# Optimization experiments

Measured on AMD Instinct MI355X. Metric: run time of the kernel, lower is better.

Reference implementation:

```python
import jax, jax.numpy as jnp
import numpy as np

N, E, IN, H, L = 50000, 640000, 64, 128, 3
EPS_DIST = 1e-8
LN_EPS = 1e-5


def setup_inputs() -> dict:
    key = jax.random.key(0)
    ks = iter(jax.random.split(key, 64))

    def rn(shape, fan_in):
        return (jax.random.normal(next(ks), shape, jnp.float32) / np.sqrt(fan_in)).astype(jnp.float32)

    inp = {}
    inp['h'] = jax.random.normal(next(ks), (N, IN), jnp.float32)
    inp['x'] = jax.random.normal(next(ks), (N, 3), jnp.float32)
    inp['edge_index'] = jax.random.randint(next(ks), (2, E), 0, N, jnp.int64)
    # embedding_in: Linear(IN, H)
    inp['W_emb'] = rn((IN, H), IN); inp['b_emb'] = jnp.zeros((H,), jnp.float32)
    # per-layer EquivariantConv params, stacked over L
    inp['Wm1'] = rn((L, 2 * H + 1, H), 2 * H + 1); inp['bm1'] = jnp.zeros((L, H), jnp.float32)
    inp['Wm2'] = rn((L, H, H), H);                 inp['bm2'] = jnp.zeros((L, H), jnp.float32)
    inp['Wc1'] = rn((L, H, H), H);                 inp['bc1'] = jnp.zeros((L, H), jnp.float32)
    inp['Wc2'] = rn((L, H, 1), H)  # no bias
    inp['Wn1'] = rn((L, 2 * H, H), 2 * H);         inp['bn1'] = jnp.zeros((L, H), jnp.float32)
    inp['Wn2'] = rn((L, H, H), H);                 inp['bn2'] = jnp.zeros((L, H), jnp.float32)
    inp['ln_g'] = jnp.ones((L, H), jnp.float32);   inp['ln_b'] = jnp.zeros((L, H), jnp.float32)
    # epsilon head params
    inp['Wem1'] = rn((2 * H + 4, H), 2 * H + 4);   inp['bem1'] = jnp.zeros((H,), jnp.float32)
    inp['Wem2'] = rn((H, H), H);                   inp['bem2'] = jnp.zeros((H,), jnp.float32)
    inp['Wec1'] = rn((H, H), H);                   inp['bec1'] = jnp.zeros((H,), jnp.float32)
    inp['Wec2'] = rn((H, 3), H);                   inp['bec2'] = jnp.zeros((3,), jnp.float32)
    inp['Wh1'] = rn((H + 3, H), H + 3);            inp['bh1'] = jnp.zeros((H,), jnp.float32)
    inp['Wh2'] = rn((H, 3), H);                    inp['bh2'] = jnp.zeros((3,), jnp.float32)
    return inp


def _layernorm(v, g, b):
    mu = jnp.mean(v, axis=-1, keepdims=True)
    var = jnp.mean((v - mu) ** 2, axis=-1, keepdims=True)
    return (v - mu) * jax.lax.rsqrt(var + LN_EPS) * g + b


def reference(h, x, edge_index, W_emb, b_emb, Wm1, bm1, Wm2, bm2, Wc1, bc1, Wc2,
              Wn1, bn1, Wn2, bn2, ln_g, ln_b, Wem1, bem1, Wem2, bem2,
              Wec1, bec1, Wec2, bec2, Wh1, bh1, Wh2, bh2):
    row, col = edge_index[0], edge_index[1]
    n = x.shape[0]
    seg = lambda v: jax.ops.segment_sum(v, col, num_segments=n)
    in_degree = seg(jnp.ones((col.shape[0], 1), x.dtype))  # [N,1]

    h = h @ W_emb + b_emb  # embedding_in

    for i in range(L):
        rel = x[row] - x[col]                                   # [E,3]
        dist = jnp.linalg.norm(rel, axis=-1, keepdims=True)     # [E,1]
        mi = jnp.concatenate([h[row], h[col], dist], axis=-1)   # [E,2H+1]
        m = jax.nn.silu(jax.nn.silu(mi @ Wm1[i] + bm1[i]) @ Wm2[i] + bm2[i])
        agg = seg(m)                                            # [N,H]
        rel_dir = rel / (dist + EPS_DIST)
        coord_mult = jnp.tanh(jax.nn.silu(m @ Wc1[i] + bc1[i]) @ Wc2[i])  # [E,1]
        coord_update = seg(coord_mult * rel_dir)                # [N,3]
        x = x + coord_update / (in_degree + 1.0)
        nu = jnp.concatenate([h, agg], axis=-1)
        h = h + jax.nn.silu(nu @ Wn1[i] + bn1[i]) @ Wn2[i] + bn2[i]
        h = _layernorm(h, ln_g[i], ln_b[i])

    # predict_epsilon (eps_directional_head=False, eps_use_local_head=True, eps_normalize_agg=False)
    rel = x[row] - x[col]
    dist = jnp.linalg.norm(rel, axis=-1, keepdims=True)
    mi = jnp.concatenate([h[row], h[col], rel, dist], axis=-1)  # [E,2H+4]
    em = jax.nn.silu(jax.nn.silu(mi @ Wem1 + bem1) @ Wem2 + bem2)
    eps_src = jax.nn.silu(em @ Wec1 + bec1) @ Wec2 + bec2       # [E,3]
    eps = seg(eps_src)                                          # [N,3]
    hx = jnp.concatenate([h, x], axis=-1)
    eps = eps + jax.nn.silu(hx @ Wh1 + bh1) @ Wh2 + bh2
    return (h, x, eps)
```

## Files before the change

kernel.cpp:

```cpp
#include <hip/hip_runtime.h>

#define N_NODES 50000
#define N_EDGES 640000
#define HDIM    128
#define NLAYERS 3

typedef __attribute__((ext_vector_type(4))) float f32x4;
typedef short s16x8 __attribute__((ext_vector_type(8)));
typedef __bf16 bf16v8 __attribute__((ext_vector_type(8)));

static __device__ __forceinline__ unsigned short f2b(float f){
  unsigned int u = __float_as_uint(f);
  unsigned int r = u + 0x7FFFu + ((u >> 16) & 1u);
  return (unsigned short)(r >> 16);
}
static __device__ __forceinline__ float b2f(unsigned short h){
  return __uint_as_float(((unsigned int)h) << 16);
}
static __device__ __forceinline__ float silu_f(float x){
  return x / (1.0f + __expf(-x));
}
static __device__ __forceinline__ unsigned int cvt2(float a, float b){
  unsigned int r;
  asm("v_cvt_pk_bf16_f32 %0, %1, %2" : "=v"(r) : "v"(a), "v"(b));
// ... 22 lines not shown
  r[4]=(short)b.x; r[5]=(short)b.y; r[6]=(short)b.z; r[7]=(short)b.w;
  return r;
}
static __device__ __forceinline__ s16x8 ldBf32(const float* __restrict__ p, int q){
  float4 a = *(const float4*)(p + (q<<2));
  float4 b = *(const float4*)(p + 16 + (q<<2));
  s16x8 r;
  r[0]=(short)f2b(a.x); r[1]=(short)f2b(a.y); r[2]=(short)f2b(a.z); r[3]=(short)f2b(a.w);
  r[4]=(short)f2b(b.x); r[5]=(short)f2b(b.y); r[6]=(short)f2b(b.z); r[7]=(short)f2b(b.w);
  return r;
}

#define GLL(SRC, DST) __builtin_amdgcn_global_load_lds( \
    (const __attribute__((address_space(1))) void*)(SRC), \
    (__attribute__((address_space(3))) void*)(DST), 16, 0, 0)
#define STG2(T0,BUF) do{ \
    const unsigned short* _s = blob + (((size_t)(T0))<<12) + (w<<11) + (lane<<3); \
    unsigned char* _d = &sm.wbuf[BUF][(w<<12) + (lane<<4)]; \
    GLL(_s, _d); GLL(_s+512, _d+1024); GLL(_s+1024, _d+2048); GLL(_s+1536, _d+3072); \
  }while(0)
#define STG1(T0,BUF) do{ \
    const unsigned short* _s = blob + (((size_t)(T0))<<12) + (w<<10) + (lane<<3); \
    unsigned char* _d = &sm.wbuf[BUF][(w<<11) + (lane<<4)]; \
    GLL(_s, _d); GLL(_s+512, _d+1024); \
  }while(0)
#define WAITV(N) asm volatile("s_waitcnt vmcnt(" #N ")" ::: "memory")
#define BARF do{ __builtin_amdgcn_s_barrier(); asm volatile("" ::: "memory"); }while(0)
#define EBAR do{ asm volatile("" ::: "memory"); __builtin_amdgcn_s_barrier(); }while(0)

#define PH2(BUF, BEXPR, ACC) do{ \
  _Pragma("unroll") for (int ti=0; ti<2; ++ti){ \
    _Pragma("unroll") for (int s=0;s<8;++s){ \
      const s16x8 _A = *(const s16x8*)&sm.wbuf[BUF][(ti<<13)+(s<<10)+toff]; \
      _Pragma("unroll") for (int e=0;e<4;++e) ACC[e][s] = MFMA(_A, (BEXPR), ACC[e][s]); \
    } } }while(0)
#define PH1(BUF, BEXPR, ACC) do{ \
  _Pragma("unroll") for (int s=0;s<8;++s){ \
    const s16x8 _A = *(const s16x8*)&sm.wbuf[BUF][(s<<10)+toff]; \
    _Pragma("unroll") for (int e=0;e<4;++e) ACC[e][s] = MFMA(_A, (BEXPR), ACC[e][s]); \
  } }while(0)

__global__ void k_conv(const float* __restrict__ W, unsigned short* __restrict__ WT, int kshift){
  const int K = 1 << kshift;
  const int idx = (blockIdx.x<<8) + threadIdx.x;
  if (idx < (K<<7)){
    const int n = idx >> kshift;
    const int k = idx & (K-1);
    WT[idx] = f2b(W[(size_t)k*HDIM + n]);
  }
}

__global__ void k_conv_blob(const float* __restrict__ W1, const float* __restrict__ W2,
                            const float* __restrict__ W3, const float* __restrict__ aux,
                            const float* __restrict__ bias, int naux,
                            unsigned short* __restrict__ blob){
  const int i = (blockIdx.x<<8) + threadIdx.x;
  if (i >= 17*4096) return;
  const int t = i >> 12;
  const int n = (i >> 5) & 127;
  const int slot = (i >> 3) & 3;
  const int j = i & 7;
  const int q = slot ^ ((n >> 1) & 3);
  const int kl = ((j >> 2) << 4) + (q << 2) + (j & 3);
  float v;
  if (t == 0)      v = (kl < naux) ? aux[(size_t)kl*HDIM + n] : (kl == 16 ? bias[n] : 0.f);
  else if (t < 9)  v = W1[(size_t)(((t-1)<<5)+kl)*HDIM + n];
  else if (t < 13) v = W2[(size_t)(((t-9)<<5)+kl)*HDIM + n];
  else             v = W3[(size_t)(((t-13)<<5)+kl)*HDIM + n];
  blob[i] = f2b(v);
}

__global__ void k_degree(const int* __restrict__ coli, int* __restrict__ degi){
  const int e = (blockIdx.x<<8) + threadIdx.x;
  if (e < N_EDGES) atomicAdd(&degi[coli[e]], 1);
}
__global__ void k_scanA(const int* __restrict__ degi, int* __restrict__ off, int* __restrict__ bsum){
  const int t = threadIdx.x, b = blockIdx.x;
  const int i = (b<<8) + t;
  const int v = (i < N_NODES) ? degi[i] : 0;
  int x = v;
  const int lane = t & 63;
  #pragma unroll
  for (int d=1; d<64; d<<=1){ int y = __shfl_up(x, d); if (lane >= d) x += y; }
  __shared__ int wsum[4];
// ... 24 lines not shown
}
__global__ void k_scanC(int* __restrict__ off, const int* __restrict__ bsum, int* __restrict__ cursor){
  const int i = (blockIdx.x<<8) + threadIdx.x;
  if (i < N_NODES){
    const int o = off[i] + bsum[i>>8];
    off[i] = o;
    cursor[i] = o;
  }
}
__global__ void k_fill(const int* __restrict__ coli, int* __restrict__ cursor, int* __restrict__ perm){
  const int e = (blockIdx.x<<8) + threadIdx.x;
  if (e < N_EDGES){
    const int p = atomicAdd(&cursor[coli[e]], 1);
    perm[e] = p;
  }
}
__global__ void k_xcopy(const float* __restrict__ xin, float* __restrict__ xbuf){
  const int i = (blockIdx.x<<8) + threadIdx.x;
  if (i < N_NODES*3) xbuf[i] = xin[i];
}

__global__ __launch_bounds__(256) void k_embed(
    const float* __restrict__ hin, const unsigned short* __restrict__ WembT,
    const float* __restrict__ bemb, float* __restrict__ hbuf,
    unsigned short* __restrict__ hb)
{
  __shared__ float s_b[128];
  const int tid = threadIdx.x;
  if (tid < 128) s_b[tid] = bemb[tid];
  __syncthreads();
  const int lane = tid & 63, q = lane>>4;
  const int n = (blockIdx.x<<6) + ((tid>>6)<<4) + (lane&15);
  const bool valid = n < N_NODES;
  const int nc = valid ? n : (N_NODES-1);
// ... 11 lines not shown
  }
  if (valid){
    float* op = hbuf + (size_t)n*HDIM;
    unsigned short* hbw = hb + (size_t)n*HDIM;
    #pragma unroll
    for (int s=0;s<8;++s){
      float4 o; o.x=acc[s][0]; o.y=acc[s][1]; o.z=acc[s][2]; o.w=acc[s][3];
      *(float4*)(op + (s<<4) + (q<<2)) = o;
      ushort4 u; u.x=f2b(o.x); u.y=f2b(o.y); u.z=f2b(o.z); u.w=f2b(o.w);
      *(ushort4*)(hbw + ((s>>1)<<5) + (q<<3) + ((s&1)<<2)) = u;
    }
  }
}

template<bool CSR>
__global__ __launch_bounds__(256,2) void k_edge_mlp(
    const unsigned short* __restrict__ hb, const float* __restrict__ xbuf,
    const int* __restrict__ rowi, const int* __restrict__ coli,
    const int* __restrict__ perm, const unsigned short* __restrict__ blob,
    const float* __restrict__ bm2v, const float* __restrict__ bc1v,
    const float* __restrict__ wc2v,
    unsigned short* __restrict__ m_buf, float* __restrict__ agg,
    float* __restrict__ cu)
{
  __shared__ struct {
    alignas(16) unsigned char wbuf[2][16384];
    int row[256], col[256], prm[256];
    float dist[256]; float rdir[256][3];
    float b2[128], bc1[128], wc2[128];
  } sm;
  const int tid = threadIdx.x, lane = tid & 63, w = tid >> 6, q = lane >> 4;
  const int q8 = q << 3;
  const int ebase = blockIdx.x << 8;
  {
    const int e = ebase + tid;
    const int r = rowi[e], c = coli[e];
    sm.row[tid] = r; sm.col[tid] = c;
    if (CSR) sm.prm[tid] = perm[e];
    const float dx = xbuf[3*r+0] - xbuf[3*c+0];
    const float dy = xbuf[3*r+1] - xbuf[3*c+1];
    const float dz = xbuf[3*r+2] - xbuf[3*c+2];
    const float d = sqrtf(dx*dx + dy*dy + dz*dz);
    sm.dist[tid] = d;
    const float inv = 1.0f / (d + 1e-8f);
    sm.rdir[tid][0] = dx*inv; sm.rdir[tid][1] = dy*inv; sm.rdir[tid][2] = dz*inv;
  }
  if (tid < 128){ sm.b2[tid]=bm2v[tid]; sm.bc1[tid]=bc1v[tid]; sm.wc2[tid]=wc2v[tid]; }
  STG2(0,0); STG2(2,1);
  __syncthreads();

  const int toff = ((lane&15)<<6) + ((q ^ ((lane>>1)&3))<<4);
  int rn[4], cn[4];
  #pragma unroll
  for (int e=0;e<4;++e){
    const int el = (w<<6) + (e<<4) + (lane&15);
    rn[e] = sm.row[el]; cn[e] = sm.col[el];
  }
  s16x8 BA[4][2], BB[4][2];
  #pragma unroll
  for (int e=0;e<4;++e){
    const int el = (w<<6) + (e<<4) + (lane&15);
    s16x8 bx = {0,0,0,0,0,0,0,0};
    if (q == 0){ bx[0] = (short)f2b(sm.dist[el]); bx[4] = (short)0x3F80; }
    BA[e][0] = bx;
    BA[e][1] = *(const s16x8*)(hb + ((size_t)rn[e]<<7) + q8);
  }
  f32x4 acc[4][8] = {};

  BARF;
  #pragma unroll
  for (int e=0;e<4;++e){
    BB[e][0] = *(const s16x8*)(hb + ((size_t)rn[e]<<7) + 32 + q8);
    BB[e][1] = *(const s16x8*)(hb + ((size_t)rn[e]<<7) + 64 + q8);
  }
  PH2(0, BA[e][ti], acc);
  EBAR; STG2(4,0);
  BARF;
  #pragma unroll
  for (int e=0;e<4;++e){
    BA[e][0] = *(const s16x8*)(hb + ((size_t)rn[e]<<7) + 96 + q8);
    BA[e][1] = *(const s16x8*)(hb + ((size_t)cn[e]<<7) + q8);
  }
  PH2(1, BB[e][ti], acc);
  EBAR; STG2(6,1);
  WAITV(12); BARF;
  #pragma unroll
  for (int e=0;e<4;++e){
    BB[e][0] = *(const s16x8*)(hb + ((size_t)cn[e]<<7) + 32 + q8);
    BB[e][1] = *(const s16x8*)(hb + ((size_t)cn[e]<<7) + 64 + q8);
  }
  PH2(0, BA[e][ti], acc);
  EBAR; STG1(8,0);
  WAITV(10); BARF;
  #pragma unroll
  for (int e=0;e<4;++e)
    BA[e][0] = *(const s16x8*)(hb + ((size_t)cn[e]<<7) + 96 + q8);
  PH2(1, BB[e][ti], acc);
  EBAR; STG2(9,1);
  WAITV(8); BARF;
  PH1(0, BA[e][0], acc);
  EBAR; STG2(11,0);

  s16x8 sb[4][4];
  #pragma unroll
  for (int e=0;e<4;++e)
    #pragma unroll
    for (int c=0;c<4;++c) sb[e][c] = siluPack(acc[e][2*c], acc[e][2*c+1]);
  f32x4 acc2[4][8];
  #pragma unroll
  for (int s=0;s<8;++s){
    const f32x4 b = *(const f32x4*)&sm.b2[(s<<4)+(q<<2)];
    #pragma unroll
    for (int e=0;e<4;++e) acc2[e][s] = b;
  }
  WAITV(4); BARF;
  PH2(1, sb[e][ti], acc2);
  EBAR; STG2(13,1);
  WAITV(4); BARF;
  PH2(0, sb[e][2+ti], acc2);
  EBAR; STG2(15,0);

  s16x8 mb[4][4];
  #pragma unroll
  for (int e=0;e<4;++e)
    #pragma unroll
    for (int c=0;c<4;++c) mb[e][c] = siluPack(acc2[e][2*c], acc2[e][2*c+1]);
  f32x4 acc3[4][8];
  #pragma unroll
  for (int s=0;s<8;++s){
    const f32x4 b = *(const f32x4*)&sm.bc1[(s<<4)+(q<<2)];
    #pragma unroll
    for (int e=0;e<4;++e) acc3[e][s] = b;
  }
  WAITV(4); BARF;
  PH2(1, mb[e][ti], acc3);
  EBAR;
  WAITV(0); BARF;
  PH2(0, mb[e][2+ti], acc3);

  float dot[4] = {0.f,0.f,0.f,0.f};
  #pragma unroll
  for (int s=0;s<8;++s){
    const f32x4 wv = *(const f32x4*)&sm.wc2[(s<<4)+(q<<2)];
    #pragma unroll
    for (int e=0;e<4;++e)
      #pragma unroll
      for (int r=0;r<4;++r) dot[e] += silu_f(acc3[e][s][r]) * wv[r];
  }
  #pragma unroll
  for (int e=0;e<4;++e){
    dot[e] += __shfl_xor(dot[e], 16);
    dot[e] += __shfl_xor(dot[e], 32);
    const float cm = tanhf(dot[e]);
    const int el = (w<<6) + (e<<4) + (lane&15);
    if (q < 3) atomicAdd(&cu[(size_t)cn[e]*3 + q], cm * sm.rdir[el][q]);
  }
  if (CSR){
    #pragma unroll
    for (int e=0;e<4;++e){
      const int el = (w<<6) + (e<<4) + (lane&15);
      unsigned short* mp = m_buf + ((size_t)sm.prm[el]<<7) + q8;
      #pragma unroll
      for (int c=0;c<4;++c) *(s16x8*)(mp + (c<<5)) = mb[e][c];
    }
  } else {
    #pragma unroll
    for (int e=0;e<4;++e){
      float* ap = agg + (size_t)cn[e]*HDIM + (q<<2);
      #pragma unroll
      for (int c=0;c<4;++c)
        #pragma unroll
        for (int j=0;j<8;++j){
          const int o = (((c<<1)+(j>>2))<<4) + (j&3);
          atomicAdd(ap + o, b2f((unsigned short)mb[e][c][j]));
        }
    }
  }
}

template<bool CSR>
__global__ __launch_bounds__(256) void k_node_mlp(
    float* __restrict__ hbuf, unsigned short* __restrict__ hb,
    float* __restrict__ xbuf,
    const unsigned short* __restrict__ m_buf, const float* __restrict__ agg,
    const int* __restrict__ off, const int* __restrict__ degi,
    const float* __restrict__ cu,
    const unsigned short* __restrict__ Wn1T, const float* __restrict__ bn1v,
    const unsigned short* __restrict__ Wn2T, const float* __restrict__ bn2v,
    const float* __restrict__ lng, const float* __restrict__ lnb)
{
  __shared__ float s_bn1[128], s_bn2[128], s_g[128], s_b[128];
  const int tid = threadIdx.x;
  const int nbase = blockIdx.x << 6;
  if (tid >= 128){
    const int f = tid - 128;
    s_bn1[f]=bn1v[f]; s_bn2[f]=bn2v[f]; s_g[f]=lng[f]; s_b[f]=lnb[f];
  } else if (tid < 64){
    const int n = nbase + tid;
    if (n < N_NODES){
      const float dd = (float)degi[n] + 1.0f;
      #pragma unroll
      for (int c=0;c<3;++c) xbuf[3*n+c] += cu[3*n+c] / dd;
    }
  }
  __syncthreads();

  const int lane = tid & 63, q = lane >> 4;
  const int q8 = q << 3;
  const int n = nbase + ((tid>>6)<<4) + (lane & 15);
  const bool valid = (n < N_NODES);
  const int nc = valid ? n : (N_NODES-1);
  const float* __restrict__ hp = hbuf + (size_t)nc*HDIM;
  const unsigned short* __restrict__ hbp = hb + (size_t)nc*HDIM;

  float aggv[4][8];
  #pragma unroll
  for (int kk=0;kk<4;++kk)
// ... 84 lines not shown
    #pragma unroll
    for (int s=0;s<8;++s){
      const int f0 = (s<<4)+(q<<2);
      float4 o;
      o.x = (v[s][0]-mu)*rs*s_g[f0+0] + s_b[f0+0];
      o.y = (v[s][1]-mu)*rs*s_g[f0+1] + s_b[f0+1];
      o.z = (v[s][2]-mu)*rs*s_g[f0+2] + s_b[f0+2];
      o.w = (v[s][3]-mu)*rs*s_g[f0+3] + s_b[f0+3];
      *(float4*)(op + f0) = o;
      ushort4 u; u.x=f2b(o.x); u.y=f2b(o.y); u.z=f2b(o.z); u.w=f2b(o.w);
      *(ushort4*)(hbw + ((s>>1)<<5) + q8 + ((s&1)<<2)) = u;
    }
  }
}

__global__ __launch_bounds__(256,2) void k_eps_edge(
    const unsigned short* __restrict__ hb, const float* __restrict__ xbuf,
    const int* __restrict__ rowi, const int* __restrict__ coli,
    const unsigned short* __restrict__ blob,
    const float* __restrict__ bem2v, const float* __restrict__ bec1v,
    const float* __restrict__ Wec2, const float* __restrict__ bec2,
    float* __restrict__ epsb)
{
  __shared__ struct {
    alignas(16) unsigned char wbuf[2][16384];
    int row[256], col[256];
    float rel[256][3]; float dist[256];
    float b2[128], bc1[128], wc[3][128];
  } sm;
  const int tid = threadIdx.x, lane = tid & 63, w = tid >> 6, q = lane >> 4;
  const int q8 = q << 3;
  const int ebase = blockIdx.x << 8;
  {
    const int e = ebase + tid;
    const int r = rowi[e], c = coli[e];
    sm.row[tid]=r; sm.col[tid]=c;
    const float dx = xbuf[3*r+0]-xbuf[3*c+0];
    const float dy = xbuf[3*r+1]-xbuf[3*c+1];
    const float dz = xbuf[3*r+2]-xbuf[3*c+2];
    sm.rel[tid][0]=dx; sm.rel[tid][1]=dy; sm.rel[tid][2]=dz;
    sm.dist[tid] = sqrtf(dx*dx+dy*dy+dz*dz);
  }
  if (tid < 128){
    sm.b2[tid]=bem2v[tid]; sm.bc1[tid]=bec1v[tid];
    sm.wc[0][tid]=Wec2[tid*3+0]; sm.wc[1][tid]=Wec2[tid*3+1]; sm.wc[2][tid]=Wec2[tid*3+2];
  }
  STG2(0,0); STG2(2,1);
  __syncthreads();

  const int toff = ((lane&15)<<6) + ((q ^ ((lane>>1)&3))<<4);
  int rn[4], cn[4];
  #pragma unroll
  for (int e=0;e<4;++e){
    const int el = (w<<6) + (e<<4) + (lane&15);
    rn[e] = sm.row[el]; cn[e] = sm.col[el];
  }
  s16x8 BA[4][2], BB[4][2];
  #pragma unroll
  for (int e=0;e<4;++e){
    const int el = (w<<6) + (e<<4) + (lane&15);
    s16x8 bx = {0,0,0,0,0,0,0,0};
    if (q == 0){
      bx[0] = (short)f2b(sm.rel[el][0]);
      bx[1] = (short)f2b(sm.rel[el][1]);
      bx[2] = (short)f2b(sm.rel[el][2]);
      bx[3] = (short)f2b(sm.dist[el]);
      bx[4] = (short)0x3F80;
    }
    BA[e][0] = bx;
    BA[e][1] = *(const s16x8*)(hb + ((size_t)rn[e]<<7) + q8);
  }
  f32x4 acc[4][8] = {};

  BARF;
  #pragma unroll
  for (int e=0;e<4;++e){
    BB[e][0] = *(const s16x8*)(hb + ((size_t)rn[e]<<7) + 32 + q8);
    BB[e][1] = *(const s16x8*)(hb + ((size_t)rn[e]<<7) + 64 + q8);
  }
  PH2(0, BA[e][ti], acc);
  EBAR; STG2(4,0);
  BARF;
  #pragma unroll
  for (int e=0;e<4;++e){
    BA[e][0] = *(const s16x8*)(hb + ((size_t)rn[e]<<7) + 96 + q8);
    BA[e][1] = *(const s16x8*)(hb + ((size_t)cn[e]<<7) + q8);
  }
  PH2(1, BB[e][ti], acc);
  EBAR; STG2(6,1);
  WAITV(12); BARF;
  #pragma unroll
  for (int e=0;e<4;++e){
    BB[e][0] = *(const s16x8*)(hb + ((size_t)cn[e]<<7) + 32 + q8);
    BB[e][1] = *(const s16x8*)(hb + ((size_t)cn[e]<<7) + 64 + q8);
  }
  PH2(0, BA[e][ti], acc);
  EBAR; STG1(8,0);
  WAITV(10); BARF;
  #pragma unroll
  for (int e=0;e<4;++e)
    BA[e][0] = *(const s16x8*)(hb + ((size_t)cn[e]<<7) + 96 + q8);
  PH2(1, BB[e][ti], acc);
  EBAR; STG2(9,1);
  WAITV(8); BARF;
  PH1(0, BA[e][0], acc);
  EBAR; STG2(11,0);

  s16x8 sb[4][4];
  #pragma unroll
  for (int e=0;e<4;++e)
    #pragma unroll
    for (int c=0;c<4;++c) sb[e][c] = siluPack(acc[e][2*c], acc[e][2*c+1]);
  f32x4 acc2[4][8];
  #pragma unroll
  for (int s=0;s<8;++s){
    const f32x4 b = *(const f32x4*)&sm.b2[(s<<4)+(q<<2)];
    #pragma unroll
    for (int e=0;e<4;++e) acc2[e][s] = b;
  }
  WAITV(4); BARF;
  PH2(1, sb[e][ti], acc2);
  EBAR; STG2(13,1);
  WAITV(4); BARF;
  PH2(0, sb[e][2+ti], acc2);
  EBAR; STG2(15,0);

  s16x8 mb[4][4];
  #pragma unroll
  for (int e=0;e<4;++e)
    #pragma unroll
    for (int c=0;c<4;++c) mb[e][c] = siluPack(acc2[e][2*c], acc2[e][2*c+1]);
  f32x4 acc3[4][8];
  #pragma unroll
  for (int s=0;s<8;++s){
    const f32x4 b = *(const f32x4*)&sm.bc1[(s<<4)+(q<<2)];
    #pragma unroll
    for (int e=0;e<4;++e) acc3[e][s] = b;
  }
  WAITV(4); BARF;
  PH2(1, mb[e][ti], acc3);
  EBAR;
  WAITV(0); BARF;
  PH2(0, mb[e][2+ti], acc3);

  float d0[4]={0,0,0,0}, d1[4]={0,0,0,0}, d2[4]={0,0,0,0};
  #pragma unroll
  for (int s=0;s<8;++s){
    const f32x4 w0 = *(const f32x4*)&sm.wc[0][(s<<4)+(q<<2)];
    const f32x4 w1 = *(const f32x4*)&sm.wc[1][(s<<4)+(q<<2)];
    const f32x4 w2 = *(const f32x4*)&sm.wc[2][(s<<4)+(q<<2)];
    #pragma unroll
    for (int e=0;e<4;++e)
      #pragma unroll
      for (int r=0;r<4;++r){
        const float ev = silu_f(acc3[e][s][r]);
        d0[e] += ev*w0[r]; d1[e] += ev*w1[r]; d2[e] += ev*w2[r];
      }
  }
  #pragma unroll
  for (int e=0;e<4;++e){
    d0[e] += __shfl_xor(d0[e],16); d0[e] += __shfl_xor(d0[e],32);
    d1[e] += __shfl_xor(d1[e],16); d1[e] += __shfl_xor(d1[e],32);
    d2[e] += __shfl_xor(d2[e],16); d2[e] += __shfl_xor(d2[e],32);
    if (q < 3){
      const float val = (q==0)?d0[e]:((q==1)?d1[e]:d2[e]);
// ... 98 lines not shown
  float* hbuf = (float*)d_out;
  float* xbuf = hbuf + (size_t)N_NODES*HDIM;
  float* epsb = xbuf + (size_t)N_NODES*3;

  char* wp = (char*)d_ws;
  auto alloc = [&](size_t bytes)->char*{
    char* p = wp; wp += (bytes + 255) & ~(size_t)255; return p;
  };
  unsigned short* WembT = (unsigned short*)alloc((size_t)128*64*2);
  unsigned short *Wn1T[NLAYERS], *Wn2T[NLAYERS];
  for (int i=0;i<NLAYERS;++i){
    Wn1T[i] = (unsigned short*)alloc((size_t)128*256*2);
    Wn2T[i] = (unsigned short*)alloc((size_t)128*128*2);
  }
  unsigned short* Wh1T  = (unsigned short*)alloc((size_t)128*128*2);
  unsigned short* blobL = (unsigned short*)alloc((size_t)NLAYERS*17*4096*2);
  unsigned short* blobE = (unsigned short*)alloc((size_t)17*4096*2);
  unsigned short* hb    = (unsigned short*)alloc((size_t)N_NODES*HDIM*2);
  int* degi   = (int*)alloc((size_t)N_NODES*4);
  int* offv   = (int*)alloc((size_t)N_NODES*4);
  int* cursor = (int*)alloc((size_t)N_NODES*4);
  int* bsum   = (int*)alloc(4096);
  float* cu   = (float*)alloc((size_t)N_NODES*3*4);
  int* perm   = (int*)alloc((size_t)N_EDGES*4);
  char* big   = alloc((size_t)N_EDGES*HDIM*2);
  const bool use_csr = ((size_t)(wp - (char*)d_ws) <= ws_size);
  unsigned short* m_buf = (unsigned short*)big;
  float* agg = (float*)big;

  auto conv = [&](const float* W, unsigned short* WT, int kshift){
    const int tot = 128 << kshift;
    k_conv<<<dim3((tot+255)/256), dim3(256), 0, stream>>>(W, WT, kshift);
  };
  conv(W_emb, WembT, 6);
  for (int i=0;i<NLAYERS;++i){
    conv(Wn1 + (size_t)i*256*128, Wn1T[i], 8);
    conv(Wn2 + (size_t)i*128*128, Wn2T[i], 7);
  }
  conv(Wh1,  Wh1T,  7);
  const int cb_grid = (17*4096)/256;
  for (int i=0;i<NLAYERS;++i){
    const float* Wm1i = Wm1 + (size_t)i*257*128;
    k_conv_blob<<<dim3(cb_grid), dim3(256), 0, stream>>>(
        Wm1i, Wm2 + (size_t)i*128*128, Wc1 + (size_t)i*128*128,
        Wm1i + (size_t)256*128, bm1 + i*128, 1, blobL + (size_t)i*17*4096);
  }
  k_conv_blob<<<dim3(cb_grid), dim3(256), 0, stream>>>(
      Wem1, Wem2, Wec1, Wem1 + (size_t)256*128, bem1, 4, blobE);

  hipMemsetAsync(degi, 0, (size_t)N_NODES*4, stream);
  k_degree<<<dim3((N_EDGES+255)/256), dim3(256), 0, stream>>>(coli, degi);
  const int nb = (N_NODES + 255)/256;
  if (use_csr){
    k_scanA<<<dim3(nb), dim3(256), 0, stream>>>(degi, offv, bsum);
    k_scanB<<<dim3(1), dim3(256), 0, stream>>>(bsum, nb);
    k_scanC<<<dim3(nb), dim3(256), 0, stream>>>(offv, bsum, cursor);
    k_fill<<<dim3((N_EDGES+255)/256), dim3(256), 0, stream>>>(coli, cursor, perm);
  }
  k_xcopy<<<dim3((N_NODES*3+255)/256), dim3(256), 0, stream>>>(x_in, xbuf);
  k_embed<<<dim3((N_NODES+63)/64), dim3(256), 0, stream>>>(h_in, WembT, b_emb, hbuf, hb);

  for (int i=0;i<NLAYERS;++i){
    hipMemsetAsync(cu, 0, (size_t)N_NODES*3*4, stream);
    if (!use_csr) hipMemsetAsync(agg, 0, (size_t)N_NODES*HDIM*4, stream);
    const unsigned short* blob_i = blobL + (size_t)i*17*4096;
    if (use_csr){
      k_edge_mlp<true><<<dim3(N_EDGES/256), dim3(256), 0, stream>>>(
        hb, xbuf, rowi, coli, perm, blob_i,
        bm2 + i*128, bc1 + i*128, Wc2 + i*128, m_buf, agg, cu);
      k_node_mlp<true><<<dim3((N_NODES+63)/64), dim3(256), 0, stream>>>(
        hbuf, hb, xbuf, m_buf, agg, offv, degi, cu,
        Wn1T[i], bn1 + i*128, Wn2T[i], bn2 + i*128, lng + i*128, lnb + i*128);
    } else {
      k_edge_mlp<false><<<dim3(N_EDGES/256), dim3(256), 0, stream>>>(
        hb, xbuf, rowi, coli, perm, blob_i,
        bm2 + i*128, bc1 + i*128, Wc2 + i*128, m_buf, agg, cu);
      k_node_mlp<false><<<dim3((N_NODES+63)/64), dim3(256), 0, stream>>>(
        hbuf, hb, xbuf, m_buf, agg, offv, degi, cu,
        Wn1T[i], bn1 + i*128, Wn2T[i], bn2 + i*128, lng + i*128, lnb + i*128);
    }
  }
  hipMemsetAsync(epsb, 0, (size_t)N_NODES*3*4, stream);
  k_eps_edge<<<dim3(N_EDGES/256), dim3(256), 0, stream>>>(
    hb, xbuf, rowi, coli, blobE, bem2, bec1, Wec2, bec2, epsb);
  k_eps_node<<<dim3((N_NODES+63)/64), dim3(256), 0, stream>>>(
    hbuf, xbuf, Wh1T, bh1, Wh1 + (size_t)128*128, Wh2, bh2, epsb);
}
```

Baseline: 1.264 ms.

## Stage full weight blob in LDS once per 512-edge block and batch setup kernels

The edge MLP kernels now load all 16 weight tiles (128 KB) into LDS in one go at block start instead of double-buffering 16 KB chunks with many barriers. Blocks grow to 512 threads covering 512 edges, so the weight staging is shared by more edges. The distance and relative-position terms become FP32 bias initialisation instead of an extra MFMA K-tile. Setup work is batched: the conversion kernels and memsets are merged into multi-job launches and an init kernel, and the node kernel clears cu after using it. The large LDS footprint limits blocks per CU, which may reduce occupancy and latency hiding for the hb gathers.

```diff
diff --git a/kernel.cpp b/kernel.cpp
--- a/kernel.cpp
+++ b/kernel.cpp
@@ -60,48 +60,25 @@
 #define GLL(SRC, DST) __builtin_amdgcn_global_load_lds( \
     (const __attribute__((address_space(1))) void*)(SRC), \
     (__attribute__((address_space(3))) void*)(DST), 16, 0, 0)
-#define STG2(T0,BUF) do{ \
-    const unsigned short* _s = blob + (((size_t)(T0))<<12) + (w<<11) + (lane<<3); \
-    unsigned char* _d = &sm.wbuf[BUF][(w<<12) + (lane<<4)]; \
-    GLL(_s, _d); GLL(_s+512, _d+1024); GLL(_s+1024, _d+2048); GLL(_s+1536, _d+3072); \
-  }while(0)
-#define STG1(T0,BUF) do{ \
-    const unsigned short* _s = blob + (((size_t)(T0))<<12) + (w<<10) + (lane<<3); \
-    unsigned char* _d = &sm.wbuf[BUF][(w<<11) + (lane<<4)]; \
-    GLL(_s, _d); GLL(_s+512, _d+1024); \
-  }while(0)
-#define WAITV(N) asm volatile("s_waitcnt vmcnt(" #N ")" ::: "memory")
-#define BARF do{ __builtin_amdgcn_s_barrier(); asm volatile("" ::: "memory"); }while(0)
-#define EBAR do{ asm volatile("" ::: "memory"); __builtin_amdgcn_s_barrier(); }while(0)
-
-#define PH2(BUF, BEXPR, ACC) do{ \
-  _Pragma("unroll") for (int ti=0; ti<2; ++ti){ \
-    _Pragma("unroll") for (int s=0;s<8;++s){ \
-      const s16x8 _A = *(const s16x8*)&sm.wbuf[BUF][(ti<<13)+(s<<10)+toff]; \
-      _Pragma("unroll") for (int e=0;e<4;++e) ACC[e][s] = MFMA(_A, (BEXPR), ACC[e][s]); \
-    } } }while(0)
-#define PH1(BUF, BEXPR, ACC) do{ \
-  _Pragma("unroll") for (int s=0;s<8;++s){ \
-    const s16x8 _A = *(const s16x8*)&sm.wbuf[BUF][(s<<10)+toff]; \
-    _Pragma("unroll") for (int e=0;e<4;++e) ACC[e][s] = MFMA(_A, (BEXPR), ACC[e][s]); \
-  } }while(0)
-
-__global__ void k_conv(const float* __restrict__ W, unsigned short* __restrict__ WT, int kshift){
-  const int K = 1 << kshift;
+
+struct ConvJob { const float* src; unsigned short* dst; int kshift; };
+struct ConvJobs { ConvJob j[8]; };
+__global__ void k_conv8(ConvJobs jobs){
+  const ConvJob jb = jobs.j[blockIdx.y];
+  const int K = 1 << jb.kshift;
   const int idx = (blockIdx.x<<8) + threadIdx.x;
   if (idx < (K<<7)){
-    const int n = idx >> kshift;
+    const int n = idx >> jb.kshift;
     const int k = idx & (K-1);
-    WT[idx] = f2b(W[(size_t)k*HDIM + n]);
-  }
-}
-
-__global__ void k_conv_blob(const float* __restrict__ W1, const float* __restrict__ W2,
-                            const float* __restrict__ W3, const float* __restrict__ aux,
-                            const float* __restrict__ bias, int naux,
-                            unsigned short* __restrict__ blob){
+    jb.dst[idx] = f2b(jb.src[(size_t)k*HDIM + n]);
+  }
+}
+
+struct BlobJob { const float *W1, *W2, *W3; unsigned short* dst; };
+struct BlobJobs { BlobJob j[4]; };
+__global__ void k_blob4(BlobJobs jobs){
+  const BlobJob jb = jobs.j[blockIdx.y];
   const int i = (blockIdx.x<<8) + threadIdx.x;
-  if (i >= 17*4096) return;
   const int t = i >> 12;
   const int n = (i >> 5) & 127;
   const int slot = (i >> 3) & 3;
@@ -109,11 +86,18 @@
   const int q = slot ^ ((n >> 1) & 3);
   const int kl = ((j >> 2) << 4) + (q << 2) + (j & 3);
   float v;
-  if (t == 0)      v = (kl < naux) ? aux[(size_t)kl*HDIM + n] : (kl == 16 ? bias[n] : 0.f);
-  else if (t < 9)  v = W1[(size_t)(((t-1)<<5)+kl)*HDIM + n];
-  else if (t < 13) v = W2[(size_t)(((t-9)<<5)+kl)*HDIM + n];
-  else             v = W3[(size_t)(((t-13)<<5)+kl)*HDIM + n];
-  blob[i] = f2b(v);
+  if (t < 8)       v = jb.W1[(size_t)((t<<5)+kl)*HDIM + n];
+  else if (t < 12) v = jb.W2[(size_t)(((t-8)<<5)+kl)*HDIM + n];
+  else             v = jb.W3[(size_t)(((t-12)<<5)+kl)*HDIM + n];
+  jb.dst[i] = f2b(v);
+}
+
+__global__ void k_init(const float* __restrict__ xin, float* __restrict__ xbuf,
+                       float* __restrict__ cu, float* __restrict__ epsb,
+                       int* __restrict__ degi){
+  const int i = (blockIdx.x<<8) + threadIdx.x;
+  if (i < N_NODES*3){ xbuf[i] = xin[i]; cu[i] = 0.f; epsb[i] = 0.f; }
+  if (i < N_NODES) degi[i] = 0;
 }
 
 __global__ void k_degree(const int* __restrict__ coli, int* __restrict__ degi){
@@ -168,10 +152,6 @@
     const int p = atomicAdd(&cursor[coli[e]], 1);
     perm[e] = p;
   }
-}
-__global__ void k_xcopy(const float* __restrict__ xin, float* __restrict__ xbuf){
-  const int i = (blockIdx.x<<8) + threadIdx.x;
-  if (i < N_NODES*3) xbuf[i] = xin[i];
 }
 
 __global__ __launch_bounds__(256) void k_embed(
@@ -213,134 +193,132 @@
 }
 
 template<bool CSR>
-__global__ __launch_bounds__(256,2) void k_edge_mlp(
+__global__ __launch_bounds__(512,2) void k_edge_mlp(
     const unsigned short* __restrict__ hb, const float* __restrict__ xbuf,
     const int* __restrict__ rowi, const int* __restrict__ coli,
     const int* __restrict__ perm, const unsigned short* __restrict__ blob,
+    const float* __restrict__ bm1v, const float* __restrict__ wm1r,
     const float* __restrict__ bm2v, const float* __restrict__ bc1v,
     const float* __restrict__ wc2v,
     unsigned short* __restrict__ m_buf, float* __restrict__ agg,
     float* __restrict__ cu)
 {
-  __shared__ struct {
-    alignas(16) unsigned char wbuf[2][16384];
-    int row[256], col[256], prm[256];
-    float dist[256]; float rdir[256][3];
-    float b2[128], bc1[128], wc2[128];
-  } sm;
-  const int tid = threadIdx.x, lane = tid & 63, w = tid >> 6, q = lane >> 4;
+  __shared__ __align__(16) unsigned char wbuf[16][8192];
+  const int tid = threadIdx.x, lane = tid & 63, q = lane >> 4;
+  const int w = tid >> 6;
   const int q8 = q << 3;
-  const int ebase = blockIdx.x << 8;
-  {
-    const int e = ebase + tid;
-    const int r = rowi[e], c = coli[e];
-    sm.row[tid] = r; sm.col[tid] = c;
-    if (CSR) sm.prm[tid] = perm[e];
-    const float dx = xbuf[3*r+0] - xbuf[3*c+0];
-    const float dy = xbuf[3*r+1] - xbuf[3*c+1];
-    const float dz = xbuf[3*r+2] - xbuf[3*c+2];
+  const int ebase = blockIdx.x << 9;
+
+  #pragma unroll
+  for (int t=0;t<16;++t)
+    GLL(blob + (t<<12) + (tid<<3), &wbuf[t][tid<<4]);
+
+  int rn[4], cn[4], pm[4];
+  float dist[4], rd0[4], rd1[4], rd2[4];
+  #pragma unroll
+  for (int e=0;e<4;++e){
+    const int ge = ebase + (w<<6) + (e<<4) + (lane&15);
+    rn[e] = rowi[ge]; cn[e] = coli[ge];
+    if (CSR) pm[e] = perm[ge];
+    const float dx = xbuf[3*rn[e]+0] - xbuf[3*cn[e]+0];
+    const float dy = xbuf[3*rn[e]+1] - xbuf[3*cn[e]+1];
+    const float dz = xbuf[3*rn[e]+2] - xbuf[3*cn[e]+2];
     const float d = sqrtf(dx*dx + dy*dy + dz*dz);
-    sm.dist[tid] = d;
+    dist[e] = d;
     const float inv = 1.0f / (d + 1e-8f);
-    sm.rdir[tid][0] = dx*inv; sm.rdir[tid][1] = dy*inv; sm.rdir[tid][2] = dz*inv;
-  }
-  if (tid < 128){ sm.b2[tid]=bm2v[tid]; sm.bc1[tid]=bc1v[tid]; sm.wc2[tid]=wc2v[tid]; }
-  STG2(0,0); STG2(2,1);
+    rd0[e] = dx*inv; rd1[e] = dy*inv; rd2[e] = dz*inv;
+  }
+
+  f32x4 acc[4][8];
+  #pragma unroll
+  for (int s=0;s<8;++s){
+    const f32x4 b1 = *(const f32x4*)&bm1v[(s<<4)+(q<<2)];
+    const f32x4 wv = *(const f32x4*)&wm1r[(s<<4)+(q<<2)];
+    #pragma unroll
+    for (int e=0;e<4;++e)
+      #pragma unroll
+      for (int r=0;r<4;++r) acc[e][s][r] = b1[r] + dist[e]*wv[r];
+  }
+  const int toff = ((lane&15)<<6) + ((q ^ ((lane>>1)&3))<<4);
+
+  s16x8 Bc[4];
+  #pragma unroll
+  for (int e=0;e<4;++e)
+    Bc[e] = *(const s16x8*)(hb + ((size_t)rn[e]<<7) + q8);
+
   __syncthreads();
 
-  const int toff = ((lane&15)<<6) + ((q ^ ((lane>>1)&3))<<4);
-  int rn[4], cn[4];
-  #pragma unroll
-  for (int e=0;e<4;++e){
-    const int el = (w<<6) + (e<<4) + (lane&15);
-    rn[e] = sm.row[el]; cn[e] = sm.col[el];
-  }
-  s16x8 BA[4][2], BB[4][2];
-  #pragma unroll
-  for (int e=0;e<4;++e){
-    const int el = (w<<6) + (e<<4) + (lane&15);
-    s16x8 bx = {0,0,0,0,0,0,0,0};
-    if (q == 0){ bx[0] = (short)f2b(sm.dist[el]); bx[4] = (short)0x3F80; }
-    BA[e][0] = bx;
-    BA[e][1] = *(const s16x8*)(hb + ((size_t)rn[e]<<7) + q8);
-  }
-  f32x4 acc[4][8] = {};
-
-  BARF;
-  #pragma unroll
-  for (int e=0;e<4;++e){
-    BB[e][0] = *(const s16x8*)(hb + ((size_t)rn[e]<<7) + 32 + q8);
-    BB[e][1] = *(const s16x8*)(hb + ((size_t)rn[e]<<7) + 64 + q8);
-  }
-  PH2(0, BA[e][ti], acc);
-  EBAR; STG2(4,0);
-  BARF;
-  #pragma unroll
-  for (int e=0;e<4;++e){
-    BA[e][0] = *(const s16x8*)(hb + ((size_t)rn[e]<<7) + 96 + q8);
-    BA[e][1] = *(const s16x8*)(hb + ((size_t)cn[e]<<7) + q8);
-  }
-  PH2(1, BB[e][ti], acc);
-  EBAR; STG2(6,1);
-  WAITV(12); BARF;
-  #pragma unroll
-  for (int e=0;e<4;++e){
-    BB[e][0] = *(const s16x8*)(hb + ((size_t)cn[e]<<7) + 32 + q8);
-    BB[e][1] = *(const s16x8*)(hb + ((size_t)cn[e]<<7) + 64 + q8);
-  }
-  PH2(0, BA[e][ti], acc);
-  EBAR; STG1(8,0);
-  WAITV(10); BARF;
+  #pragma unroll
+  for (int kk=0;kk<8;++kk){
+    s16x8 Bn[4];
+    if (kk < 7){
+      const int k1 = kk+1;
+      #pragma unroll
+      for (int e=0;e<4;++e){
+        const int node = (k1 < 4) ? rn[e] : cn[e];
+        Bn[e] = *(const s16x8*)(hb + ((size_t)node<<7) + ((k1&3)<<5) + q8);
+      }
+    }
+    #pragma unroll
+    for (int s=0;s<8;++s){
+      const s16x8 A = *(const s16x8*)&wbuf[kk][(s<<10)+toff];
+      #pragma unroll
+      for (int e=0;e<4;++e) acc[e][s] = MFMA(A, Bc[e], acc[e][s]);
+    }
+    if (kk < 7){
+      #pragma unroll
+      for (int e=0;e<4;++e) Bc[e] = Bn[e];
+    }
+  }
+
+  s16x8 sb[4][4];
   #pragma unroll
   for (int e=0;e<4;++e)
-    BA[e][0] = *(const s16x8*)(hb + ((size_t)cn[e]<<7) + 96 + q8);
-  PH2(1, BB[e][ti], acc);
-  EBAR; STG2(9,1);
-  WAITV(8); BARF;
-  PH1(0, BA[e][0], acc);
-  EBAR; STG2(11,0);
-
-  s16x8 sb[4][4];
+    #pragma unroll
+    for (int c=0;c<4;++c) sb[e][c] = siluPack(acc[e][2*c], acc[e][2*c+1]);
+
+  f32x4 acc2[4][8];
+  #pragma unroll
+  for (int s=0;s<8;++s){
+    const f32x4 b = *(const f32x4*)&bm2v[(s<<4)+(q<<2)];
+    #pragma unroll
+    for (int e=0;e<4;++e) acc2[e][s] = b;
+  }
+  #pragma unroll
+  for (int c=0;c<4;++c)
+    #pragma unroll
+    for (int s=0;s<8;++s){
+      const s16x8 A = *(const s16x8*)&wbuf[8+c][(s<<10)+toff];
+      #pragma unroll
+      for (int e=0;e<4;++e) acc2[e][s] = MFMA(A, sb[e][c], acc2[e][s]);
+    }
+
+  s16x8 mb[4][4];
   #pragma unroll
   for (int e=0;e<4;++e)
     #pragma unroll
-    for (int c=0;c<4;++c) sb[e][c] = siluPack(acc[e][2*c], acc[e][2*c+1]);
-  f32x4 acc2[4][8];
+    for (int c=0;c<4;++c) mb[e][c] = siluPack(acc2[e][2*c], acc2[e][2*c+1]);
+
+  f32x4 acc3[4][8];
   #pragma unroll
   for (int s=0;s<8;++s){
-    const f32x4 b = *(const f32x4*)&sm.b2[(s<<4)+(q<<2)];
-    #pragma unroll
-    for (int e=0;e<4;++e) acc2[e][s] = b;
-  }
-  WAITV(4); BARF;
-  PH2(1, sb[e][ti], acc2);
-  EBAR; STG2(13,1);
-  WAITV(4); BARF;
-  PH2(0, sb[e][2+ti], acc2);
-  EBAR; STG2(15,0);
-
-  s16x8 mb[4][4];
-  #pragma unroll
-  for (int e=0;e<4;++e)
-    #pragma unroll
-    for (int c=0;c<4;++c) mb[e][c] = siluPack(acc2[e][2*c], acc2[e][2*c+1]);
-  f32x4 acc3[4][8];
+    const f32x4 b = *(const f32x4*)&bc1v[(s<<4)+(q<<2)];
+    #pragma unroll
+    for (int e=0;e<4;++e) acc3[e][s] = b;
+  }
+  #pragma unroll
+  for (int c=0;c<4;++c)
+    #pragma unroll
+    for (int s=0;s<8;++s){
+      const s16x8 A = *(const s16x8*)&wbuf[12+c][(s<<10)+toff];
+      #pragma unroll
+      for (int e=0;e<4;++e) acc3[e][s] = MFMA(A, mb[e][c], acc3[e][s]);
+    }
+
+  float dot[4] = {0.f,0.f,0.f,0.f};
   #pragma unroll
   for (int s=0;s<8;++s){
-    const f32x4 b = *(const f32x4*)&sm.bc1[(s<<4)+(q<<2)];
-    #pragma unroll
-    for (int e=0;e<4;++e) acc3[e][s] = b;
-  }
-  WAITV(4); BARF;
-  PH2(1, mb[e][ti], acc3);
-  EBAR;
-  WAITV(0); BARF;
-  PH2(0, mb[e][2+ti], acc3);
-
-  float dot[4] = {0.f,0.f,0.f,0.f};
-  #pragma unroll
-  for (int s=0;s<8;++s){
-    const f32x4 wv = *(const f32x4*)&sm.wc2[(s<<4)+(q<<2)];
+    const f32x4 wv = *(const f32x4*)&wc2v[(s<<4)+(q<<2)];
     #pragma unroll
     for (int e=0;e<4;++e)
       #pragma unroll
@@ -351,14 +329,15 @@
     dot[e] += __shfl_xor(dot[e], 16);
     dot[e] += __shfl_xor(dot[e], 32);
     const float cm = tanhf(dot[e]);
-    const int el = (w<<6) + (e<<4) + (lane&15);
-    if (q < 3) atomicAdd(&cu[(size_t)cn[e]*3 + q], cm * sm.rdir[el][q]);
+    if (q < 3){
+      const float rdq = (q==0) ? rd0[e] : ((q==1) ? rd1[e] : rd2[e]);
+      atomicAdd(&cu[(size_t)cn[e]*3 + q], cm * rdq);
+    }
   }
   if (CSR){
     #pragma unroll
     for (int e=0;e<4;++e){
-      const int el = (w<<6) + (e<<4) + (lane&15);
-      unsigned short* mp = m_buf + ((size_t)sm.prm[el]<<7) + q8;
+      unsigned short* mp = m_buf + ((size_t)pm[e]<<7) + q8;
       #pragma unroll
       for (int c=0;c<4;++c) *(s16x8*)(mp + (c<<5)) = mb[e][c];
     }
@@ -383,7 +362,7 @@
     float* __restrict__ xbuf,
     const unsigned short* __restrict__ m_buf, const float* __restrict__ agg,
     const int* __restrict__ off, const int* __restrict__ degi,
-    const float* __restrict__ cu,
+    float* __restrict__ cu,
     const unsigned short* __restrict__ Wn1T, const float* __restrict__ bn1v,
     const unsigned short* __restrict__ Wn2T, const float* __restrict__ bn2v,
     const float* __restrict__ lng, const float* __restrict__ lnb)
@@ -399,7 +378,10 @@
     if (n < N_NODES){
       const float dd = (float)degi[n] + 1.0f;
       #pragma unroll
-      for (int c=0;c<3;++c) xbuf[3*n+c] += cu[3*n+c] / dd;
+      for (int c=0;c<3;++c){
+        xbuf[3*n+c] += cu[3*n+c] / dd;
+        cu[3*n+c] = 0.f;
+      }
     }
   }
   __syncthreads();
@@ -514,141 +496,142 @@
   }
 }
 
-__global__ __launch_bounds__(256,2) void k_eps_edge(
+__global__ __launch_bounds__(512,2) void k_eps_edge(
     const unsigned short* __restrict__ hb, const float* __restrict__ xbuf,
     const int* __restrict__ rowi, const int* __restrict__ coli,
     const unsigned short* __restrict__ blob,
+    const float* __restrict__ bem1v, const float* __restrict__ wem_rows,
     const float* __restrict__ bem2v, const float* __restrict__ bec1v,
     const float* __restrict__ Wec2, const float* __restrict__ bec2,
     float* __restrict__ epsb)
 {
-  __shared__ struct {
-    alignas(16) unsigned char wbuf[2][16384];
-    int row[256], col[256];
-    float rel[256][3]; float dist[256];
-    float b2[128], bc1[128], wc[3][128];
-  } sm;
-  const int tid = threadIdx.x, lane = tid & 63, w = tid >> 6, q = lane >> 4;
+  __shared__ __align__(16) unsigned char wbuf[16][8192];
+  __shared__ float wcs[3][128];
+  const int tid = threadIdx.x, lane = tid & 63, q = lane >> 4;
+  const int w = tid >> 6;
   const int q8 = q << 3;
-  const int ebase = blockIdx.x << 8;
-  {
-    const int e = ebase + tid;
-    const int r = rowi[e], c = coli[e];
-    sm.row[tid]=r; sm.col[tid]=c;
-    const float dx = xbuf[3*r+0]-xbuf[3*c+0];
-    const float dy = xbuf[3*r+1]-xbuf[3*c+1];
-    const float dz = xbuf[3*r+2]-xbuf[3*c+2];
-    sm.rel[tid][0]=dx; sm.rel[tid][1]=dy; sm.rel[tid][2]=dz;
-    sm.dist[tid] = sqrtf(dx*dx+dy*dy+dz*dz);
-  }
+  const int ebase = blockIdx.x << 9;
+
+  #pragma unroll
+  for (int t=0;t<16;++t)
+    GLL(blob + (t<<12) + (tid<<3), &wbuf[t][tid<<4]);
   if (tid < 128){
-    sm.b2[tid]=bem2v[tid]; sm.bc1[tid]=bec1v[tid];
-    sm.wc[0][tid]=Wec2[tid*3+0]; sm.wc[1][tid]=Wec2[tid*3+1]; sm.wc[2][tid]=Wec2[tid*3+2];
-  }
-  STG2(0,0); STG2(2,1);
+    wcs[0][tid] = Wec2[tid*3+0];
+    wcs[1][tid] = Wec2[tid*3+1];
+    wcs[2][tid] = Wec2[tid*3+2];
+  }
+
+  int rn[4], cn[4];
+  float rl0[4], rl1[4], rl2[4], dist[4];
+  #pragma unroll
+  for (int e=0;e<4;++e){
+    const int ge = ebase + (w<<6) + (e<<4) + (lane&15);
+    rn[e] = rowi[ge]; cn[e] = coli[ge];
+    const float dx = xbuf[3*rn[e]+0] - xbuf[3*cn[e]+0];
+    const float dy = xbuf[3*rn[e]+1] - xbuf[3*cn[e]+1];
+    const float dz = xbuf[3*rn[e]+2] - xbuf[3*cn[e]+2];
+    rl0[e]=dx; rl1[e]=dy; rl2[e]=dz;
+    dist[e] = sqrtf(dx*dx + dy*dy + dz*dz);
+  }
+
+  f32x4 acc[4][8];
+  #pragma unroll
+  for (int s=0;s<8;++s){
+    const int f4 = (s<<4)+(q<<2);
+    const f32x4 b1 = *(const f32x4*)&bem1v[f4];
+    const f32x4 w0 = *(const f32x4*)&wem_rows[f4];
+    const f32x4 w1 = *(const f32x4*)&wem_rows[128+f4];
+    const f32x4 w2 = *(const f32x4*)&wem_rows[256+f4];
+    const f32x4 w3 = *(const f32x4*)&wem_rows[384+f4];
+    #pragma unroll
+    for (int e=0;e<4;++e)
+      #pragma unroll
+      for (int r=0;r<4;++r)
+        acc[e][s][r] = b1[r] + rl0[e]*w0[r] + rl1[e]*w1[r] + rl2[e]*w2[r] + dist[e]*w3[r];
+  }
+  const int toff = ((lane&15)<<6) + ((q ^ ((lane>>1)&3))<<4);
+
+  s16x8 Bc[4];
+  #pragma unroll
+  for (int e=0;e<4;++e)
+    Bc[e] = *(const s16x8*)(hb + ((size_t)rn[e]<<7) + q8);
+
   __syncthreads();
 
-  const int toff = ((lane&15)<<6) + ((q ^ ((lane>>1)&3))<<4);
-  int rn[4], cn[4];
-  #pragma unroll
-  for (int e=0;e<4;++e){
-    const int el = (w<<6) + (e<<4) + (lane&15);
-    rn[e] = sm.row[el]; cn[e] = sm.col[el];
-  }
-  s16x8 BA[4][2], BB[4][2];
-  #pragma unroll
-  for (int e=0;e<4;++e){
-    const int el = (w<<6) + (e<<4) + (lane&15);
-    s16x8 bx = {0,0,0,0,0,0,0,0};
-    if (q == 0){
-      bx[0] = (short)f2b(sm.rel[el][0]);
-      bx[1] = (short)f2b(sm.rel[el][1]);
-      bx[2] = (short)f2b(sm.rel[el][2]);
-      bx[3] = (short)f2b(sm.dist[el]);
-      bx[4] = (short)0x3F80;
-    }
-    BA[e][0] = bx;
-    BA[e][1] = *(const s16x8*)(hb + ((size_t)rn[e]<<7) + q8);
-  }
-  f32x4 acc[4][8] = {};
-
-  BARF;
-  #pragma unroll
-  for (int e=0;e<4;++e){
-    BB[e][0] = *(const s16x8*)(hb + ((size_t)rn[e]<<7) + 32 + q8);
-    BB[e][1] = *(const s16x8*)(hb + ((size_t)rn[e]<<7) + 64 + q8);
-  }
-  PH2(0, BA[e][ti], acc);
-  EBAR; STG2(4,0);
-  BARF;
-  #pragma unroll
-  for (int e=0;e<4;++e){
-    BA[e][0] = *(const s16x8*)(hb + ((size_t)rn[e]<<7) + 96 + q8);
-    BA[e][1] = *(const s16x8*)(hb + ((size_t)cn[e]<<7) + q8);
-  }
-  PH2(1, BB[e][ti], acc);
-  EBAR; STG2(6,1);
-  WAITV(12); BARF;
-  #pragma unroll
-  for (int e=0;e<4;++e){
-    BB[e][0] = *(const s16x8*)(hb + ((size_t)cn[e]<<7) + 32 + q8);
-    BB[e][1] = *(const s16x8*)(hb + ((size_t)cn[e]<<7) + 64 + q8);
-  }
-  PH2(0, BA[e][ti], acc);
-  EBAR; STG1(8,0);
-  WAITV(10); BARF;
+  #pragma unroll
+  for (int kk=0;kk<8;++kk){
+    s16x8 Bn[4];
+    if (kk < 7){
+      const int k1 = kk+1;
+      #pragma unroll
+      for (int e=0;e<4;++e){
+        const int node = (k1 < 4) ? rn[e] : cn[e];
+        Bn[e] = *(const s16x8*)(hb + ((size_t)node<<7) + ((k1&3)<<5) + q8);
+      }
+    }
+    #pragma unroll
+    for (int s=0;s<8;++s){
+      const s16x8 A = *(const s16x8*)&wbuf[kk][(s<<10)+toff];
+      #pragma unroll
+      for (int e=0;e<4;++e) acc[e][s] = MFMA(A, Bc[e], acc[e][s]);
+    }
+    if (kk < 7){
+      #pragma unroll
+      for (int e=0;e<4;++e) Bc[e] = Bn[e];
+    }
+  }
+
+  s16x8 sb[4][4];
   #pragma unroll
   for (int e=0;e<4;++e)
-    BA[e][0] = *(const s16x8*)(hb + ((size_t)cn[e]<<7) + 96 + q8);
-  PH2(1, BB[e][ti], acc);
-  EBAR; STG2(9,1);
-  WAITV(8); BARF;
-  PH1(0, BA[e][0], acc);
-  EBAR; STG2(11,0);
-
-  s16x8 sb[4][4];
+    #pragma unroll
+    for (int c=0;c<4;++c) sb[e][c] = siluPack(acc[e][2*c], acc[e][2*c+1]);
+
+  f32x4 acc2[4][8];
+  #pragma unroll
+  for (int s=0;s<8;++s){
+    const f32x4 b = *(const f32x4*)&bem2v[(s<<4)+(q<<2)];
+    #pragma unroll
+    for (int e=0;e<4;++e) acc2[e][s] = b;
+  }
+  #pragma unroll
+  for (int c=0;c<4;++c)
+    #pragma unroll
+    for (int s=0;s<8;++s){
+      const s16x8 A = *(const s16x8*)&wbuf[8+c][(s<<10)+toff];
+      #pragma unroll
+      for (int e=0;e<4;++e) acc2[e][s] = MFMA(A, sb[e][c], acc2[e][s]);
+    }
+
+  s16x8 mb[4][4];
   #pragma unroll
   for (int e=0;e<4;++e)
     #pragma unroll
-    for (int c=0;c<4;++c) sb[e][c] = siluPack(acc[e][2*c], acc[e][2*c+1]);
-  f32x4 acc2[4][8];
+    for (int c=0;c<4;++c) mb[e][c] = siluPack(acc2[e][2*c], acc2[e][2*c+1]);
+
+  f32x4 acc3[4][8];
   #pragma unroll
   for (int s=0;s<8;++s){
-    const f32x4 b = *(const f32x4*)&sm.b2[(s<<4)+(q<<2)];
-    #pragma unroll
-    for (int e=0;e<4;++e) acc2[e][s] = b;
-  }
-  WAITV(4); BARF;
-  PH2(1, sb[e][ti], acc2);
-  EBAR; STG2(13,1);
-  WAITV(4); BARF;
-  PH2(0, sb[e][2+ti], acc2);
-  EBAR; STG2(15,0);
-
-  s16x8 mb[4][4];
-  #pragma unroll
-  for (int e=0;e<4;++e)
-    #pragma unroll
-    for (int c=0;c<4;++c) mb[e][c] = siluPack(acc2[e][2*c], acc2[e][2*c+1]);
-  f32x4 acc3[4][8];
+    const f32x4 b = *(const f32x4*)&bec1v[(s<<4)+(q<<2)];
+    #pragma unroll
+    for (int e=0;e<4;++e) acc3[e][s] = b;
+  }
+  #pragma unroll
+  for (int c=0;c<4;++c)
+    #pragma unroll
+    for (int s=0;s<8;++s){
+      const s16x8 A = *(const s16x8*)&wbuf[12+c][(s<<10)+toff];
+      #pragma unroll
+      for (int e=0;e<4;++e) acc3[e][s] = MFMA(A, mb[e][c], acc3[e][s]);
+    }
+
+  float d0[4]={0,0,0,0}, d1[4]={0,0,0,0}, d2[4]={0,0,0,0};
   #pragma unroll
   for (int s=0;s<8;++s){
-    const f32x4 b = *(const f32x4*)&sm.bc1[(s<<4)+(q<<2)];
-    #pragma unroll
-    for (int e=0;e<4;++e) acc3[e][s] = b;
-  }
-  WAITV(4); BARF;
-  PH2(1, mb[e][ti], acc3);
-  EBAR;
-  WAITV(0); BARF;
-  PH2(0, mb[e][2+ti], acc3);
-
-  float d0[4]={0,0,0,0}, d1[4]={0,0,0,0}, d2[4]={0,0,0,0};
-  #pragma unroll
-  for (int s=0;s<8;++s){
-    const f32x4 w0 = *(const f32x4*)&sm.wc[0][(s<<4)+(q<<2)];
-    const f32x4 w1 = *(const f32x4*)&sm.wc[1][(s<<4)+(q<<2)];
-    const f32x4 w2 = *(const f32x4*)&sm.wc[2][(s<<4)+(q<<2)];
+    const int f4 = (s<<4)+(q<<2);
+    const f32x4 w0 = *(const f32x4*)&wcs[0][f4];
+    const f32x4 w1 = *(const f32x4*)&wcs[1][f4];
+    const f32x4 w2 = *(const f32x4*)&wcs[2][f4];
     #pragma unroll
     for (int e=0;e<4;++e)
       #pragma unroll
@@ -777,8 +760,8 @@
     Wn2T[i] = (unsigned short*)alloc((size_t)128*128*2);
   }
   unsigned short* Wh1T  = (unsigned short*)alloc((size_t)128*128*2);
-  unsigned short* blobL = (unsigned short*)alloc((size_t)NLAYERS*17*4096*2);
-  unsigned short* blobE = (unsigned short*)alloc((size_t)17*4096*2);
+  unsigned short* blobL = (unsigned short*)alloc((size_t)NLAYERS*16*4096*2);
+  unsigned short* blobE = (unsigned short*)alloc((size_t)16*4096*2);
   unsigned short* hb    = (unsigned short*)alloc((size_t)N_NODES*HDIM*2);
   int* degi   = (int*)alloc((size_t)N_NODES*4);
   int* offv   = (int*)alloc((size_t)N_NODES*4);
@@ -791,27 +774,24 @@
   unsigned short* m_buf = (unsigned short*)big;
   float* agg = (float*)big;
 
-  auto conv = [&](const float* W, unsigned short* WT, int kshift){
-    const int tot = 128 << kshift;
-    k_conv<<<dim3((tot+255)/256), dim3(256), 0, stream>>>(W, WT, kshift);
-  };
-  conv(W_emb, WembT, 6);
+  ConvJobs cj;
+  cj.j[0] = {W_emb, WembT, 6};
   for (int i=0;i<NLAYERS;++i){
-    conv(Wn1 + (size_t)i*256*128, Wn1T[i], 8);
-    conv(Wn2 + (size_t)i*128*128, Wn2T[i], 7);
-  }
-  conv(Wh1,  Wh1T,  7);
-  const int cb_grid = (17*4096)/256;
-  for (int i=0;i<NLAYERS;++i){
-    const float* Wm1i = Wm1 + (size_t)i*257*128;
-    k_conv_blob<<<dim3(cb_grid), dim3(256), 0, stream>>>(
-        Wm1i, Wm2 + (size_t)i*128*128, Wc1 + (size_t)i*128*128,
-        Wm1i + (size_t)256*128, bm1 + i*128, 1, blobL + (size_t)i*17*4096);
-  }
-  k_conv_blob<<<dim3(cb_grid), dim3(256), 0, stream>>>(
-      Wem1, Wem2, Wec1, Wem1 + (size_t)256*128, bem1, 4, blobE);
-
-  hipMemsetAsync(degi, 0, (size_t)N_NODES*4, stream);
+    cj.j[1+i] = {Wn1 + (size_t)i*256*128, Wn1T[i], 8};
+    cj.j[4+i] = {Wn2 + (size_t)i*128*128, Wn2T[i], 7};
+  }
+  cj.j[7] = {Wh1, Wh1T, 7};
+  k_conv8<<<dim3(128,8), dim3(256), 0, stream>>>(cj);
+
+  BlobJobs bj;
+  for (int i=0;i<NLAYERS;++i)
+    bj.j[i] = {Wm1 + (size_t)i*257*128, Wm2 + (size_t)i*128*128,
+               Wc1 + (size_t)i*128*128, blobL + (size_t)i*16*4096};
+  bj.j[3] = {Wem1, Wem2, Wec1, blobE};
+  k_blob4<<<dim3(256,4), dim3(256), 0, stream>>>(bj);
+
+  k_init<<<dim3((N_NODES*3+255)/256), dim3(256), 0, stream>>>(x_in, xbuf, cu, epsb, degi);
+
   k_degree<<<dim3((N_EDGES+255)/256), dim3(256), 0, stream>>>(coli, degi);
   const int nb = (N_NODES + 255)/256;
   if (use_csr){
@@ -820,32 +800,33 @@
     k_scanC<<<dim3(nb), dim3(256), 0, stream>>>(offv, bsum, cursor);
     k_fill<<<dim3((N_EDGES+255)/256), dim3(256), 0, stream>>>(coli, cursor, perm);
   }
-  k_xcopy<<<dim3((N_NODES*3+255)/256), dim3(256), 0, stream>>>(x_in, xbuf);
   k_embed<<<dim3((N_NODES+63)/64), dim3(256), 0, stream>>>(h_in, WembT, b_emb, hbuf, hb);
 
   for (int i=0;i<NLAYERS;++i){
-    hipMemsetAsync(cu, 0, (size_t)N_NODES*3*4, stream);
     if (!use_csr) hipMemsetAsync(agg, 0, (size_t)N_NODES*HDIM*4, stream);
-    const unsigned short* blob_i = blobL + (size_t)i*17*4096;
+    const unsigned short* blob_i = blobL + (size_t)i*16*4096;
+    const float* wm1r = Wm1 + (size_t)i*257*128 + (size_t)256*128;
     if (use_csr){
-      k_edge_mlp<true><<<dim3(N_EDGES/256), dim3(256), 0, stream>>>(
+      k_edge_mlp<true><<<dim3(N_EDGES/512), dim3(512), 0, stream>>>(
         hb, xbuf, rowi, coli, perm, blob_i,
-        bm2 + i*128, bc1 + i*128, Wc2 + i*128, m_buf, agg, cu);
+        bm1 + i*128, wm1r, bm2 + i*128, bc1 + i*128, Wc2 + i*128,
+        m_buf, agg, cu);
       k_node_mlp<true><<<dim3((N_NODES+63)/64), dim3(256), 0, stream>>>(
         hbuf, hb, xbuf, m_buf, agg, offv, degi, cu,
         Wn1T[i], bn1 + i*128, Wn2T[i], bn2 + i*128, lng + i*128, lnb + i*128);
     } else {
-      k_edge_mlp<false><<<dim3(N_EDGES/256), dim3(256), 0, stream>>>(
+      k_edge_mlp<false><<<dim3(N_EDGES/512), dim3(512), 0, stream>>>(
         hb, xbuf, rowi, coli, perm, blob_i,
-        bm2 + i*128, bc1 + i*128, Wc2 + i*128, m_buf, agg, cu);
+        bm1 + i*128, wm1r, bm2 + i*128, bc1 + i*128, Wc2 + i*128,
+        m_buf, agg, cu);
       k_node_mlp<false><<<dim3((N_NODES+63)/64), dim3(256), 0, stream>>>(
         hbuf, hb, xbuf, m_buf, agg, offv, degi, cu,
         Wn1T[i], bn1 + i*128, Wn2T[i], bn2 + i*128, lng + i*128, lnb + i*128);
     }
   }
-  hipMemsetAsync(epsb, 0, (size_t)N_NODES*3*4, stream);
-  k_eps_edge<<<dim3(N_EDGES/256), dim3(256), 0, stream>>>(
-    hb, xbuf, rowi, coli, blobE, bem2, bec1, Wec2, bec2, epsb);
+  k_eps_edge<<<dim3(N_EDGES/512), dim3(512), 0, stream>>>(
+    hb, xbuf, rowi, coli, blobE,
+    bem1, Wem1 + (size_t)256*128, bem2, bec1, Wec2, bec2, epsb);
   k_eps_node<<<dim3((N_NODES+63)/64), dim3(256), 0, stream>>>(
     hbuf, xbuf, Wh1T, bh1, Wh1 + (size_t)128*128, Wh2, bh2, epsb);
 }
```

Measured after the change: 1.436 ms. +13.7%, slower.
